# Performance work log

Measured on AMD Instinct MI355X. Metric: run time of the kernel, lower is better.

The kernel has to match this reference:

```python
import jax, jax.numpy as jnp
import numpy as np

N = 100000
D = 512


def setup_inputs() -> dict:
    key = jax.random.key(0)
    k1, k2 = jax.random.split(key)
    features = jax.random.normal(k1, (N, D), dtype=jnp.float32)
    attn_w = jax.random.normal(k2, (D,), dtype=jnp.float32)
    attn_b = jnp.zeros((1,), dtype=jnp.float32)
    return {"features": features, "attn_w": attn_w, "attn_b": attn_b, "k": 4}


def reference(features, attn_w, attn_b, k):
    # features: [N, D]; sliding-window (half-width k, truncated at edges) mean
    n = features.shape[0]
    zero = jnp.zeros((1, features.shape[1]), dtype=features.dtype)
    cs = jnp.concatenate([zero, jnp.cumsum(features, axis=0)], axis=0)  # [N+1, D]
    i = jnp.arange(n)
    lo = jnp.maximum(i - k, 0)          # inclusive window start
    hi = jnp.minimum(i + k, n - 1)      # inclusive window end
    win_sum = cs[hi + 1] - cs[lo]       # [N, D]
    count = (hi - lo + 1).astype(features.dtype)[:, None]
    agg = win_sum / count               # [N, D] windowed means
    scores = agg @ attn_w + attn_b[0]   # [N]
    w = jax.nn.softmax(scores, axis=0)  # [N]
    bag = w @ agg                       # [D]
    return bag, w
```

## Files before the change

kernel.cpp:

```cpp
#include <hip/hip_runtime.h>
#include <math.h>

#define D 512
#define NB_P 1000
#define OWN 128
#define HALOA 8

__device__ __forceinline__ float dot4(float4 a, float4 b) {
    return a.x*b.x + a.y*b.y + a.z*b.z + a.w*b.w;
}

__global__ __launch_bounds__(256) void k_a(
    const float* __restrict__ f, const float* __restrict__ w,
    const float* __restrict__ bptr, const int* __restrict__ kptr,
    float* __restrict__ e_out, float* __restrict__ uu,
    float* __restrict__ psum, int n)
{
    __shared__ float dots[OWN + 2 * HALOA];
    __shared__ float e_sh[OWN + 2 * HALOA];
    __shared__ float sm[4];
    int lane = threadIdx.x & 63;
    int wid  = threadIdx.x >> 6;
    int t    = threadIdx.x;
    int g0   = blockIdx.x * OWN - HALOA;

    const float4* wr = (const float4*)w;
    float4 b0 = wr[lane], b1 = wr[lane + 64];

    for (int lr = wid; lr < OWN + 2 * HALOA; lr += 4) {
        int row = g0 + lr;
        bool v = (row >= 0) && (row < n);
        const float4* fr = (const float4*)(f + (size_t)(v ? row : 0) * D);
        float4 a0 = fr[lane], a1 = fr[lane + 64];
        float s = dot4(a0, b0) + dot4(a1, b1);
        #pragma unroll
        for (int off = 32; off; off >>= 1) s += __shfl_down(s, off);
        if (lane == 0) dots[lr] = v ? s : 0.f;
    }
    __syncthreads();

    int k = *kptr;
    float bias = bptr[0];

    float e_reg = 0.f;
    if (t < OWN + 2 * HALOA) {
        int i = g0 + t;
        if (t >= HALOA - k && t < HALOA + OWN + k && i >= 0 && i < n) {
            int lo = max(i - k, 0), hi = min(i + k, n - 1);
            float s = 0.f;
            for (int q = lo; q <= hi; ++q) s += dots[q - g0];
            e_reg = __expf(s / (float)(hi - lo + 1) + bias);
        }
        e_sh[t] = e_reg;
    }
    __syncthreads();

    float pv = (t >= HALOA && t < HALOA + OWN) ? e_reg : 0.f;
    #pragma unroll
    for (int off = 32; off; off >>= 1) pv += __shfl_down(pv, off);
    if (lane == 0) sm[wid] = pv;
    __syncthreads();
    if (t == 0) psum[blockIdx.x] = sm[0] + sm[1] + sm[2] + sm[3];

    if (t < OWN) {
        int j = blockIdx.x * OWN + t;
        if (j < n) {
            e_out[j] = e_sh[t + HALOA];
            int lo = max(j - k, 0), hi = min(j + k, n - 1);
            float acc = 0.f;
            for (int i = lo; i <= hi; ++i) {
                int li = max(i - k, 0), hh = min(i + k, n - 1);
                acc += e_sh[i - g0] * __builtin_amdgcn_rcpf((float)(hh - li + 1));
            }
            uu[j] = acc;
        }
    }
}

__global__ void k_pbag(const float* __restrict__ f, const float* __restrict__ u,
                       float* __restrict__ partial, int n, int chunk) {
    int t = threadIdx.x;
    int j0 = blockIdx.x * chunk;
    int j1 = min(j0 + chunk, n);
    float4 acc0 = make_float4(0.f,0.f,0.f,0.f);
    float4 acc1 = make_float4(0.f,0.f,0.f,0.f);
    float4 acc2 = make_float4(0.f,0.f,0.f,0.f);
    float4 acc3 = make_float4(0.f,0.f,0.f,0.f);
    int j = j0;
    for (; j + 4 <= j1; j += 4) {
        float u0 = u[j], u1 = u[j+1], u2 = u[j+2], u3 = u[j+3];
        float4 v0 = ((const float4*)(f + (size_t)(j  ) * D))[t];
        float4 v1 = ((const float4*)(f + (size_t)(j+1) * D))[t];
        float4 v2 = ((const float4*)(f + (size_t)(j+2) * D))[t];
        float4 v3 = ((const float4*)(f + (size_t)(j+3) * D))[t];
        acc0.x += u0*v0.x; acc0.y += u0*v0.y; acc0.z += u0*v0.z; acc0.w += u0*v0.w;
        acc1.x += u1*v1.x; acc1.y += u1*v1.y; acc1.z += u1*v1.z; acc1.w += u1*v1.w;
        acc2.x += u2*v2.x; acc2.y += u2*v2.y; acc2.z += u2*v2.z; acc2.w += u2*v2.w;
        acc3.x += u3*v3.x; acc3.y += u3*v3.y; acc3.z += u3*v3.z; acc3.w += u3*v3.w;
    }
    for (; j < j1; ++j) {
        float uj = u[j];
        float4 v = ((const float4*)(f + (size_t)j * D))[t];
        acc0.x += uj*v.x; acc0.y += uj*v.y; acc0.z += uj*v.z; acc0.w += uj*v.w;
    }
    float4 a;
    a.x = (acc0.x + acc1.x) + (acc2.x + acc3.x);
    a.y = (acc0.y + acc1.y) + (acc2.y + acc3.y);
    a.z = (acc0.z + acc1.z) + (acc2.z + acc3.z);
    a.w = (acc0.w + acc1.w) + (acc2.w + acc3.w);
    ((float4*)(partial + (size_t)blockIdx.x * D))[t] = a;
}

__global__ void k_final(const float* __restrict__ partial, const float* __restrict__ psum,
                        int nbp, int nbs, const float* __restrict__ e,
                        float* __restrict__ bag, float* __restrict__ w_out, int n) {
    __shared__ float sm[4];
    __shared__ float ginv;
    int lane = threadIdx.x & 63, wid = threadIdx.x >> 6;

    float s = 0.f;
    for (int idx = threadIdx.x; idx < nbs; idx += 256) s += psum[idx];
    #pragma unroll
    for (int off = 32; off; off >>= 1) s += __shfl_down(s, off);
    if (lane == 0) sm[wid] = s;
    __syncthreads();
    if (threadIdx.x == 0)
        ginv = 1.f / (sm[0] + sm[1] + sm[2] + sm[3]);
    __syncthreads();
    float inv = ginv;

    if (blockIdx.x < 32) {
        int c = blockIdx.x * 16 + (threadIdx.x & 15);
        int r = threadIdx.x >> 4;
        float acc = 0.f;
        for (int b = r; b < nbp; b += 16) acc += partial[(size_t)b * D + c];
        __shared__ float sred[256];
        sred[threadIdx.x] = acc;
        __syncthreads();
        if (threadIdx.x < 16) {
            float tt = 0.f;
            #pragma unroll
            for (int q = 0; q < 16; ++q) tt += sred[q * 16 + threadIdx.x];
            bag[blockIdx.x * 16 + threadIdx.x] = tt * inv;
        }
    }

    for (int j = blockIdx.x * 256 + threadIdx.x; j < n; j += gridDim.x * 256)
        w_out[j] = e[j] * inv;
}

extern "C" void kernel_launch(void* const* d_in, const int* in_sizes, int n_in,
                              void* d_out, int out_size, void* d_ws, size_t ws_size,
                              hipStream_t stream) {
    const float* f  = (const float*)d_in[0];
    const float* aw = (const float*)d_in[1];
    const float* ab = (const float*)d_in[2];
    const int*   kp = (const int*)d_in[3];
    int n = in_sizes[0] / D;

    float* bag   = (float*)d_out;
    float* w_out = (float*)d_out + D;

    int nbA = (n + OWN - 1) / OWN;
    int nb2 = (n + 255) / 256;

    float* wsf     = (float*)d_ws;
    float* e       = wsf;
    float* uu      = wsf + n;
    float* psum    = wsf + 2 * (size_t)n;
    size_t poff    = ((2 * (size_t)n + (size_t)nbA) + 31) & ~(size_t)31;
    float* partial = wsf + poff;

    int chunk = (n + NB_P - 1) / NB_P;

    k_a    <<<nbA, 256, 0, stream>>>(f, aw, ab, kp, e, uu, psum, n);
    k_pbag <<<NB_P, 128, 0, stream>>>(f, uu, partial, n, chunk);
    k_final<<<nb2, 256, 0, stream>>>(partial, psum, NB_P, nbA, e, bag, w_out, n);
}
```

Measured before the change: 89.47 us.

## Fuse weighted feature accumulation into the score kernel using shared per-block weights

Merges the score/exp kernel and the weighted-bag partial-sum kernel into one. Each block keeps its per-row window weights in shared memory and immediately re-reads the same 128 feature rows it just dotted with the attention vector. Those rows are then likely still in cache, which removes the second full pass over the features, the global uu buffer and one launch. In exchange, only half the threads do the accumulation phase, and the final kernel must reduce more, smaller partials (one per block).

```diff
diff --git a/kernel.cpp b/kernel.cpp
--- a/kernel.cpp
+++ b/kernel.cpp
@@ -2,7 +2,6 @@
 #include <math.h>
 
 #define D 512
-#define NB_P 1000
 #define OWN 128
 #define HALOA 8
 
@@ -10,14 +9,15 @@
     return a.x*b.x + a.y*b.y + a.z*b.z + a.w*b.w;
 }
 
-__global__ __launch_bounds__(256) void k_a(
+__global__ __launch_bounds__(256) void k_ab(
     const float* __restrict__ f, const float* __restrict__ w,
     const float* __restrict__ bptr, const int* __restrict__ kptr,
-    float* __restrict__ e_out, float* __restrict__ uu,
-    float* __restrict__ psum, int n)
+    float* __restrict__ e_out, float* __restrict__ psum,
+    float* __restrict__ partial, int n)
 {
     __shared__ float dots[OWN + 2 * HALOA];
     __shared__ float e_sh[OWN + 2 * HALOA];
+    __shared__ float uu_sh[OWN];
     __shared__ float sm[4];
     int lane = threadIdx.x & 63;
     int wid  = threadIdx.x >> 6;
@@ -64,51 +64,51 @@
 
     if (t < OWN) {
         int j = blockIdx.x * OWN + t;
+        float acc = 0.f;
         if (j < n) {
             e_out[j] = e_sh[t + HALOA];
             int lo = max(j - k, 0), hi = min(j + k, n - 1);
-            float acc = 0.f;
             for (int i = lo; i <= hi; ++i) {
                 int li = max(i - k, 0), hh = min(i + k, n - 1);
                 acc += e_sh[i - g0] * __builtin_amdgcn_rcpf((float)(hh - li + 1));
             }
-            uu[j] = acc;
         }
+        uu_sh[t] = acc;
     }
-}
+    __syncthreads();
 
-__global__ void k_pbag(const float* __restrict__ f, const float* __restrict__ u,
-                       float* __restrict__ partial, int n, int chunk) {
-    int t = threadIdx.x;
-    int j0 = blockIdx.x * chunk;
-    int j1 = min(j0 + chunk, n);
-    float4 acc0 = make_float4(0.f,0.f,0.f,0.f);
-    float4 acc1 = make_float4(0.f,0.f,0.f,0.f);
-    float4 acc2 = make_float4(0.f,0.f,0.f,0.f);
-    float4 acc3 = make_float4(0.f,0.f,0.f,0.f);
-    int j = j0;
-    for (; j + 4 <= j1; j += 4) {
-        float u0 = u[j], u1 = u[j+1], u2 = u[j+2], u3 = u[j+3];
-        float4 v0 = ((const float4*)(f + (size_t)(j  ) * D))[t];
-        float4 v1 = ((const float4*)(f + (size_t)(j+1) * D))[t];
-        float4 v2 = ((const float4*)(f + (size_t)(j+2) * D))[t];
-        float4 v3 = ((const float4*)(f + (size_t)(j+3) * D))[t];
-        acc0.x += u0*v0.x; acc0.y += u0*v0.y; acc0.z += u0*v0.z; acc0.w += u0*v0.w;
-        acc1.x += u1*v1.x; acc1.y += u1*v1.y; acc1.z += u1*v1.z; acc1.w += u1*v1.w;
-        acc2.x += u2*v2.x; acc2.y += u2*v2.y; acc2.z += u2*v2.z; acc2.w += u2*v2.w;
-        acc3.x += u3*v3.x; acc3.y += u3*v3.y; acc3.z += u3*v3.z; acc3.w += u3*v3.w;
+    if (t < 128) {
+        int j0 = blockIdx.x * OWN;
+        int j1 = min(j0 + OWN, n);
+        float4 acc0 = make_float4(0.f,0.f,0.f,0.f);
+        float4 acc1 = make_float4(0.f,0.f,0.f,0.f);
+        float4 acc2 = make_float4(0.f,0.f,0.f,0.f);
+        float4 acc3 = make_float4(0.f,0.f,0.f,0.f);
+        int j = j0;
+        for (; j + 4 <= j1; j += 4) {
+            int lr = j - j0;
+            float u0 = uu_sh[lr], u1 = uu_sh[lr+1], u2 = uu_sh[lr+2], u3 = uu_sh[lr+3];
+            float4 v0 = ((const float4*)(f + (size_t)(j  ) * D))[t];
+            float4 v1 = ((const float4*)(f + (size_t)(j+1) * D))[t];
+            float4 v2 = ((const float4*)(f + (size_t)(j+2) * D))[t];
+            float4 v3 = ((const float4*)(f + (size_t)(j+3) * D))[t];
+            acc0.x += u0*v0.x; acc0.y += u0*v0.y; acc0.z += u0*v0.z; acc0.w += u0*v0.w;
+            acc1.x += u1*v1.x; acc1.y += u1*v1.y; acc1.z += u1*v1.z; acc1.w += u1*v1.w;
+            acc2.x += u2*v2.x; acc2.y += u2*v2.y; acc2.z += u2*v2.z; acc2.w += u2*v2.w;
+            acc3.x += u3*v3.x; acc3.y += u3*v3.y; acc3.z += u3*v3.z; acc3.w += u3*v3.w;
+        }
+        for (; j < j1; ++j) {
+            float uj = uu_sh[j - j0];
+            float4 v = ((const float4*)(f + (size_t)j * D))[t];
+            acc0.x += uj*v.x; acc0.y += uj*v.y; acc0.z += uj*v.z; acc0.w += uj*v.w;
+        }
+        float4 a;
+        a.x = (acc0.x + acc1.x) + (acc2.x + acc3.x);
+        a.y = (acc0.y + acc1.y) + (acc2.y + acc3.y);
+        a.z = (acc0.z + acc1.z) + (acc2.z + acc3.z);
+        a.w = (acc0.w + acc1.w) + (acc2.w + acc3.w);
+        ((float4*)(partial + (size_t)blockIdx.x * D))[t] = a;
     }
-    for (; j < j1; ++j) {
-        float uj = u[j];
-        float4 v = ((const float4*)(f + (size_t)j * D))[t];
-        acc0.x += uj*v.x; acc0.y += uj*v.y; acc0.z += uj*v.z; acc0.w += uj*v.w;
-    }
-    float4 a;
-    a.x = (acc0.x + acc1.x) + (acc2.x + acc3.x);
-    a.y = (acc0.y + acc1.y) + (acc2.y + acc3.y);
-    a.z = (acc0.z + acc1.z) + (acc2.z + acc3.z);
-    a.w = (acc0.w + acc1.w) + (acc2.w + acc3.w);
-    ((float4*)(partial + (size_t)blockIdx.x * D))[t] = a;
 }
 
 __global__ void k_final(const float* __restrict__ partial, const float* __restrict__ psum,
@@ -166,14 +166,10 @@
 
     float* wsf     = (float*)d_ws;
     float* e       = wsf;
-    float* uu      = wsf + n;
-    float* psum    = wsf + 2 * (size_t)n;
-    size_t poff    = ((2 * (size_t)n + (size_t)nbA) + 31) & ~(size_t)31;
+    float* psum    = wsf + n;
+    size_t poff    = (((size_t)n + (size_t)nbA) + 31) & ~(size_t)31;
     float* partial = wsf + poff;
 
-    int chunk = (n + NB_P - 1) / NB_P;
-
-    k_a    <<<nbA, 256, 0, stream>>>(f, aw, ab, kp, e, uu, psum, n);
-    k_pbag <<<NB_P, 128, 0, stream>>>(f, uu, partial, n, chunk);
-    k_final<<<nb2, 256, 0, stream>>>(partial, psum, NB_P, nbA, e, bag, w_out, n);
+    k_ab   <<<nbA, 256, 0, stream>>>(f, aw, ab, kp, e, psum, partial, n);
+    k_final<<<nb2, 256, 0, stream>>>(partial, psum, nbA, nbA, e, bag, w_out, n);
 }
```

Result: faster. 81.98 us, median of 2 (-8.4%).
